# Performance work log

Measured on AMD Instinct MI355X. Metric: run time of the kernel, lower is better.

## Reference

```python
import jax, jax.numpy as jnp
from jax import lax
import numpy as np

H = 16  # GRU hidden = 4**N_GRAM * 4
V = 4   # 4**N_GRAM
B = 512
S = 8192


def _gru_cell(x, h, Wih, Whh, bih, bhh):
    # PyTorch GRU gate ordering: r, z, n
    gi = x @ Wih.T + bih          # [B, 3H]
    gh = h @ Whh.T + bhh          # [B, 3H]
    ir, iz, inn = jnp.split(gi, 3, axis=-1)
    hr, hz, hn = jnp.split(gh, 3, axis=-1)
    r = jax.nn.sigmoid(ir + hr)
    z = jax.nn.sigmoid(iz + hz)
    n = jnp.tanh(inn + r * hn)
    return (1.0 - z) * n + z * h


def setup_inputs() -> dict:
    key = jax.random.key(0)
    ks = jax.random.split(key, 12)
    f32 = jnp.float32
    k_i = 1.0 / np.sqrt(H)  # torch default GRU/Linear init scale
    u = lambda k, shp: jax.random.uniform(k, shp, f32, -k_i, k_i)
    gt = jax.random.normal(ks[0], (B, V, S), f32)
    return {
        "ground_truth": gt,
        "enc_Wih": u(ks[1], (3 * H, V)),
        "enc_Whh": u(ks[2], (3 * H, H)),
        "enc_bih": u(ks[3], (3 * H,)),
        "enc_bhh": u(ks[4], (3 * H,)),
        "dec_Wih": u(ks[5], (3 * H, V)),
        "dec_Whh": u(ks[6], (3 * H, H)),
        "dec_bih": u(ks[7], (3 * H,)),
        "dec_bhh": u(ks[8], (3 * H,)),
        "out_W": u(ks[9], (V, H)),
        "out_b": u(ks[10], (V,)),
        "emb": jnp.eye(V, dtype=f32),  # one-hot Embedding_LUT (frozen)
        "tf_rate": 1,
    }


def reference(ground_truth, enc_Wih, enc_Whh, enc_bih, enc_bhh,
              dec_Wih, dec_Whh, dec_bih, dec_bhh, out_W, out_b, emb, tf_rate):
    gt = jnp.transpose(ground_truth, (2, 0, 1))      # [S, B, V]
    seq_l, batch, _ = gt.shape
    dt = gt.dtype
    h0 = jnp.zeros((batch, H), dt)

    def enc_step(h, x):
        return _gru_cell(x, h, enc_Wih, enc_Whh, enc_bih, enc_bhh), None
    enc_hidden, _ = lax.scan(enc_step, h0, gt)

    targets = jnp.argmax(gt, axis=2)                 # [S, B] int
    x0 = jnp.zeros((batch, V), dt)
    loss0 = jnp.asarray(0.0, dt)

    if tf_rate >= 1:  # argmax-feedback branch (random() < tf_rate always true)
        def dec_step(carry, tgt):
            x, h, loss = carry
            h = _gru_cell(x, h, dec_Wih, dec_Whh, dec_bih, dec_bhh)
            out = h @ out_W.T + out_b                # [B, V]
            logp = jax.nn.log_softmax(out, axis=-1)
            nll = -jnp.mean(jnp.take_along_axis(logp, tgt[:, None], axis=1))
            top_i = jnp.argmax(out, axis=-1)
            return (emb[top_i], h, loss + nll), None
        (_, _, loss), _ = lax.scan(dec_step, (x0, enc_hidden, loss0), targets)
        output_batch = jnp.zeros((seq_l, batch, V), dt)  # never written in this branch
    else:  # teacher-forcing branch (NLLLoss applied to raw logits, as in source)
        def dec_step(carry, inp):
            x, h, loss = carry
            gt_t, tgt = inp
            h = _gru_cell(x, h, dec_Wih, dec_Whh, dec_bih, dec_bhh)
            out = h @ out_W.T + out_b
            nll = -jnp.mean(jnp.take_along_axis(out, tgt[:, None], axis=1))
            return (gt_t, h, loss + nll), out
        (_, _, loss), output_batch = lax.scan(dec_step, (x0, enc_hidden, loss0), (gt, targets))

    return loss, jnp.transpose(output_batch, (1, 2, 0))  # [B, V, S]
```

## Files before the change

### kernel.cpp

```cpp
#include <hip/hip_runtime.h>

#define S_LEN 8192
#define NH 16
#define NV 4
#define NB 512

typedef _Float16 h2 __attribute__((ext_vector_type(2)));

template<int R>
__device__ __forceinline__ float rotf(float v) {
    return __int_as_float(__builtin_amdgcn_mov_dpp(__float_as_int(v), 0x120 + R, 0xF, 0xF, true));
}
template<int R>
__device__ __forceinline__ h2 roth(h2 v) {
    int i;
    __builtin_memcpy(&i, &v, 4);
    i = __builtin_amdgcn_mov_dpp(i, 0x120 + R, 0xF, 0xF, true);
    h2 o;
    __builtin_memcpy(&o, &i, 4);
    return o;
}
__device__ __forceinline__ float qxor1(float v) {
    return __int_as_float(__builtin_amdgcn_mov_dpp(__float_as_int(v), 0xB1, 0xF, 0xF, true));
}
__device__ __forceinline__ float qxor2(float v) {
    return __int_as_float(__builtin_amdgcn_mov_dpp(__float_as_int(v), 0x4E, 0xF, 0xF, true));
}

__device__ __forceinline__ float fsig(float x) {
    return __builtin_amdgcn_rcpf(1.0f + __expf(-x));
}
__device__ __forceinline__ float frcp(float x) { return __builtin_amdgcn_rcpf(x); }
__device__ __forceinline__ float4 ld4(const float* p) { return *(const float4*)p; }

__device__ __forceinline__ h2 pkh(float a, float b) {
    auto t = __builtin_amdgcn_cvt_pkrtz(a, b);
    h2 o;
    __builtin_memcpy(&o, &t, 4);
    return o;
}

__device__ __forceinline__ float xor32f(float v, bool isLo) {
    float a = v, b = v;
    asm("v_permlane32_swap_b32 %0, %1" : "+v"(a), "+v"(b));
    return isLo ? b : a;
}

#define FILL_HP16(hp, h)                                      \
    do {                                                      \
        h2 p0_ = pkh((h), rotf<1>(h));                        \
        hp[0] = p0_;                                          \
        hp[1] = roth<2>(p0_);                                 \
        hp[2] = roth<4>(p0_);                                 \
        hp[3] = roth<6>(p0_);                                 \
        hp[4] = roth<8>(p0_);                                 \
        hp[5] = roth<10>(p0_);                                \
        hp[6] = roth<12>(p0_);                                \
        hp[7] = roth<14>(p0_);                                \
    } while (0)

__device__ __forceinline__ float dotd2(const h2* __restrict__ w, const h2* hp, float start) {
    float a = __builtin_amdgcn_fdot2(w[0], hp[0], start, false);
    float b = __builtin_amdgcn_fdot2(w[1], hp[1], 0.0f, false);
    a = __builtin_amdgcn_fdot2(w[2], hp[2], a, false);
    b = __builtin_amdgcn_fdot2(w[3], hp[3], b, false);
    a = __builtin_amdgcn_fdot2(w[4], hp[4], a, false);
    b = __builtin_amdgcn_fdot2(w[5], hp[5], b, false);
    a = __builtin_amdgcn_fdot2(w[6], hp[6], a, false);
    b = __builtin_amdgcn_fdot2(w[7], hp[7], b, false);
    return a + b;
}

__global__ __launch_bounds__(64, 1) void enc_kernel(
    const float* __restrict__ gt,
    const float* __restrict__ eWih, const float* __restrict__ eWhh,
    const float* __restrict__ ebih, const float* __restrict__ ebhh,
    float* __restrict__ hsc)
{
    const int lane = threadIdx.x;
    const int j    = lane & 15;
    const int b    = blockIdx.x * 4 + (lane >> 4);

    int probe = __builtin_amdgcn_mov_dpp(j, 0x121, 0xF, 0xF, true);
    const int sgn = (probe == ((j + 1) & 15)) ? 1 : -1;

    const float* gb = gt + (size_t)b * (NV * S_LEN);

    h2 ewr[8], ewz[8], ewn[8];
#pragma unroll
    for (int p = 0; p < 8; ++p) {
        int k0 = (j + sgn * (2 * p)) & 15;
        int k1 = (j + sgn * (2 * p + 1)) & 15;
        ewr[p] = (h2){(_Float16)eWhh[(0 * NH + j) * NH + k0], (_Float16)eWhh[(0 * NH + j) * NH + k1]};
        ewz[p] = (h2){(_Float16)eWhh[(1 * NH + j) * NH + k0], (_Float16)eWhh[(1 * NH + j) * NH + k1]};
        ewn[p] = (h2){(_Float16)eWhh[(2 * NH + j) * NH + k0], (_Float16)eWhh[(2 * NH + j) * NH + k1]};
    }
    float exr[NV], exz[NV], exn[NV];
#pragma unroll
    for (int v = 0; v < NV; ++v) {
        exr[v] = eWih[(0 * NH + j) * NV + v];
        exz[v] = eWih[(1 * NH + j) * NV + v];
        exn[v] = eWih[(2 * NH + j) * NV + v];
    }
    const float c_er  = ebih[j] + ebhh[j];
    const float c_ez  = ebih[NH + j] + ebhh[NH + j];
    const float c_ein = ebih[2 * NH + j];
    const float c_ehn = ebhh[2 * NH + j];

    float h = 0.0f;

    auto gru = [&](float ar, float az, float hn, float inn) {
        float r  = fsig(ar);
        float z  = fsig(az);
        float t2 = fmaf(-2.0f, z, 2.0f);
        float tb = fmaf(z, h, z - 1.0f);
        float y  = fmaf(r, hn, inn);
        float w2 = frcp(1.0f + __expf(-2.0f * y));
        h = fmaf(w2, t2, tb);
    };

    auto estep = [&](float x0, float x1, float x2, float x3) {
        float xr = fmaf(exr[0], x0, fmaf(exr[1], x1, fmaf(exr[2], x2, fmaf(exr[3], x3, c_er))));
        float xz = fmaf(exz[0], x0, fmaf(exz[1], x1, fmaf(exz[2], x2, fmaf(exz[3], x3, c_ez))));
        float xn = fmaf(exn[0], x0, fmaf(exn[1], x1, fmaf(exn[2], x2, fmaf(exn[3], x3, c_ein))));
        h2 hp[8];
        FILL_HP16(hp, h);
        float ar = dotd2(ewr, hp, xr);
        float az = dotd2(ewz, hp, xz);
        float hn = dotd2(ewn, hp, c_ehn);
        gru(ar, az, hn, xn);
    };

    {
        float4 A0 = ld4(gb + 0 * S_LEN), A1 = ld4(gb + 1 * S_LEN),
               A2 = ld4(gb + 2 * S_LEN), A3 = ld4(gb + 3 * S_LEN);
        float4 B0 = ld4(gb + 0 * S_LEN + 4), B1 = ld4(gb + 1 * S_LEN + 4),
               B2 = ld4(gb + 2 * S_LEN + 4), B3 = ld4(gb + 3 * S_LEN + 4);
        for (int t = 0; t < S_LEN; t += 8) {
            estep(A0.x, A1.x, A2.x, A3.x);
            estep(A0.y, A1.y, A2.y, A3.y);
            estep(A0.z, A1.z, A2.z, A3.z);
            estep(A0.w, A1.w, A2.w, A3.w);
            int ta = t + 8;  if (ta > S_LEN - 4) ta = S_LEN - 4;
            A0 = ld4(gb + 0 * S_LEN + ta); A1 = ld4(gb + 1 * S_LEN + ta);
            A2 = ld4(gb + 2 * S_LEN + ta); A3 = ld4(gb + 3 * S_LEN + ta);
            estep(B0.x, B1.x, B2.x, B3.x);
            estep(B0.y, B1.y, B2.y, B3.y);
            estep(B0.z, B1.z, B2.z, B3.z);
            estep(B0.w, B1.w, B2.w, B3.w);
            int tb2 = t + 12; if (tb2 > S_LEN - 4) tb2 = S_LEN - 4;
            B0 = ld4(gb + 0 * S_LEN + tb2); B1 = ld4(gb + 1 * S_LEN + tb2);
            B2 = ld4(gb + 2 * S_LEN + tb2); B3 = ld4(gb + 3 * S_LEN + tb2);
        }
    }

    hsc[(size_t)b * NH + j] = h;
}

__global__ __launch_bounds__(64, 1) void dec_kernel(
    const float* __restrict__ dWih, const float* __restrict__ dWhh,
    const float* __restrict__ dbih, const float* __restrict__ dbhh,
    const float* __restrict__ oW,  const float* __restrict__ ob,
    const float* __restrict__ hsc,
    float* __restrict__ outs)
{
    const int lane = threadIdx.x;
    const int j    = lane & 15;
    const int q    = j & 3;
    const int row  = lane >> 4;
    const bool isLo = (lane < 32);
    const int b    = blockIdx.x * 2 + (row & 1);

    int probe = __builtin_amdgcn_mov_dpp(j, 0x121, 0xF, 0xF, true);
    const int sgn = (probe == ((j + 1) & 15)) ? 1 : -1;

    const int gA = isLo ? 0 : 1;
    h2 wA[8], wB[8];
#pragma unroll
    for (int p = 0; p < 8; ++p) {
        int k0 = (j + sgn * (2 * p)) & 15;
        int k1 = (j + sgn * (2 * p + 1)) & 15;
        wA[p] = (h2){(_Float16)dWhh[(gA * NH + j) * NH + k0],
                     (_Float16)dWhh[(gA * NH + j) * NH + k1]};
        float w0 = isLo ? dWhh[(2 * NH + j) * NH + k0] : oW[q * NH + k0];
        float w1 = isLo ? dWhh[(2 * NH + j) * NH + k1] : oW[q * NH + k1];
        wB[p] = (h2){(_Float16)w0, (_Float16)w1};
    }
    const float bR  = dbih[j] + dbhh[j];
    const float bZ  = dbih[NH + j] + dbhh[NH + j];
    const float bNi = dbih[2 * NH + j];
    const float bHn = dbhh[2 * NH + j];
    const float biasA  = isLo ? bR  : bZ;
    const float startB = isLo ? bHn : ob[q];
    float SA[NV], KN[NV];
#pragma unroll
    for (int m = 0; m < NV; ++m) {
        int c = m ^ q;
        SA[m] = dWih[(gA * NH + j) * NV + c];
        KN[m] = bNi + dWih[(2 * NH + j) * NV + c];
    }

    float h = hsc[(size_t)b * NH + j];

    int oidx = (b << 15) + q;
    const bool storer = isLo && (j < 4);

    auto dstep = [&]() {
        h2 hp[8];
        FILL_HP16(hp, h);
        float aA  = dotd2(wA, hp, biasA);
        float aB  = dotd2(wB, hp, startB);
        float aBP = xor32f(aB, isLo);
        float hn  = isLo ? aB  : aBP;
        float oa  = isLo ? aBP : aB;
        if (storer) outs[oidx] = oa;
        oidx += 4;
        float ob_ = qxor1(oa);
        float oc_ = qxor2(oa);
        float od_ = qxor2(ob_);
        bool cA = ob_ > oa;  float mA = fmaxf(oa, ob_);
        bool cB = od_ > oc_; float mB = fmaxf(oc_, od_);
        bool hi_ = mB > mA;
        float KA  = hi_ ? (cB ? SA[3] : SA[2]) : (cA ? SA[1] : SA[0]);
        float KN_ = hi_ ? (cB ? KN[3] : KN[2]) : (cA ? KN[1] : KN[0]);
        float sg  = fsig(aA + KA);
        float sgP = xor32f(sg, isLo);
        float r   = isLo ? sg  : sgP;
        float z   = isLo ? sgP : sg;
        float y   = fmaf(r, hn, KN_);
        float w2  = frcp(1.0f + __expf(-2.0f * y));
        float t2  = fmaf(-2.0f, z, 2.0f);
        float tb  = fmaf(z, h, z - 1.0f);
        h = fmaf(w2, t2, tb);
    };

    {
        h2 hp[8];
        FILL_HP16(hp, h);
        float aA  = dotd2(wA, hp, biasA);
        float aB  = dotd2(wB, hp, startB);
        float aBP = xor32f(aB, isLo);
        float hn  = isLo ? aB : aBP;
        float sg  = fsig(aA);
        float sgP = xor32f(sg, isLo);
        float r   = isLo ? sg  : sgP;
        float z   = isLo ? sgP : sg;
        float y   = fmaf(r, hn, bNi);
        float w2  = frcp(1.0f + __expf(-2.0f * y));
        float t2  = fmaf(-2.0f, z, 2.0f);
        float tb  = fmaf(z, h, z - 1.0f);
        h = fmaf(w2, t2, tb);
    }
    for (int u = 0; u < S_LEN - 4; u += 4) {
        dstep(); dstep(); dstep(); dstep();
    }
    dstep(); dstep(); dstep();

    {
        h2 hp[8];
        FILL_HP16(hp, h);
        float aB  = dotd2(wB, hp, startB);
        float aBP = xor32f(aB, isLo);
        float oa  = isLo ? aBP : aB;
        if (storer) outs[oidx] = oa;
    }
}

__global__ __launch_bounds__(1024) void loss_kernel(
    const float* __restrict__ gt, float* __restrict__ outs, float* __restrict__ loss)
{
    int tid = blockIdx.x * 1024 + threadIdx.x;
    int t = tid & (S_LEN - 1);
    int b = tid >> 13;
    float4 o = *(const float4*)(outs + (size_t)tid * 4);
    const float* g = gt + (size_t)b * (NV * S_LEN) + t;
    float p0 = g[0], p1 = g[S_LEN], p2 = g[2 * S_LEN], p3 = g[3 * S_LEN];
    int tg = (p1 > p0) ? 1 : 0;  float bm = fmaxf(p0, p1);
    tg = (p2 > bm) ? 2 : tg;     bm = fmaxf(p2, bm);
    tg = (p3 > bm) ? 3 : tg;
    float vt = (tg & 1) ? ((tg & 2) ? o.w : o.y) : ((tg & 2) ? o.z : o.x);
    float mx = fmaxf(fmaxf(o.x, o.y), fmaxf(o.z, o.w));
    float ss = __expf(o.x - mx) + __expf(o.y - mx) + __expf(o.z - mx) + __expf(o.w - mx);
    float v  = (mx - vt) + __logf(ss);
    *(float4*)(outs + (size_t)tid * 4) = make_float4(0.f, 0.f, 0.f, 0.f);
#pragma unroll
    for (int d = 1; d < 64; d <<= 1) v += __shfl_xor(v, d, 64);
    __shared__ float sm[16];
    int w = threadIdx.x >> 6;
    if ((threadIdx.x & 63) == 0) sm[w] = v;
    __syncthreads();
    if (threadIdx.x < 16) {
        float s = sm[threadIdx.x];
#pragma unroll
        for (int d = 1; d < 16; d <<= 1) s += __shfl_xor(s, d, 64);
        if (threadIdx.x == 0) atomicAdd(loss, s * (1.0f / NB));
    }
}

extern "C" void kernel_launch(void* const* d_in, const int* in_sizes, int n_in,
                              void* d_out, int out_size, void* d_ws, size_t ws_size,
                              hipStream_t stream) {
    (void)in_sizes; (void)n_in; (void)ws_size; (void)out_size;
    const float* gt   = (const float*)d_in[0];
    const float* eWih = (const float*)d_in[1];
    const float* eWhh = (const float*)d_in[2];
    const float* ebih = (const float*)d_in[3];
    const float* ebhh = (const float*)d_in[4];
    const float* dWih = (const float*)d_in[5];
    const float* dWhh = (const float*)d_in[6];
    const float* dbih = (const float*)d_in[7];
    const float* dbhh = (const float*)d_in[8];
    const float* oW   = (const float*)d_in[9];
    const float* ob   = (const float*)d_in[10];

    float* out  = (float*)d_out;
    float* outs = out + 1;
    float* hsc  = (float*)d_ws;
    (void)hipMemsetAsync(d_out, 0, sizeof(float), stream);
    enc_kernel<<<NB / 4, 64, 0, stream>>>(gt, eWih, eWhh, ebih, ebhh, hsc);
    dec_kernel<<<NB / 2, 64, 0, stream>>>(dWih, dWhh, dbih, dbhh, oW, ob, hsc, outs);
    loss_kernel<<<(NB * S_LEN) / 1024, 1024, 0, stream>>>(gt, outs, out);
}
```

Measured before the change: 3.329 ms.

## Split encoder gates across wave halves and fold log2e into weights for exp2

The encoder now handles two batch rows per 64-lane wave instead of four. The low half computes the r gate and the hidden part of the n gate, and the high half computes the z gate and the input part of the n gate, exchanging results with a permlane32 swap. Input projections are folded into the fp16 dot products as extra packed lanes. Both kernels pre-scale weights by log2(e) so sigmoid and tanh use exp2 directly, removing a multiply from the serial recurrence. This doubles the encoder wave count and puts the input projection into fp16, which costs some precision.

```diff
diff --git a/kernel.cpp b/kernel.cpp
--- a/kernel.cpp
+++ b/kernel.cpp
@@ -6,6 +6,9 @@
 #define NB 512
 
 typedef _Float16 h2 __attribute__((ext_vector_type(2)));
+
+#define L2E  1.4426950408889634f
+#define L2E2 2.8853900817779268f
 
 template<int R>
 __device__ __forceinline__ float rotf(float v) {
@@ -27,10 +30,9 @@
     return __int_as_float(__builtin_amdgcn_mov_dpp(__float_as_int(v), 0x4E, 0xF, 0xF, true));
 }
 
-__device__ __forceinline__ float fsig(float x) {
-    return __builtin_amdgcn_rcpf(1.0f + __expf(-x));
-}
+__device__ __forceinline__ float fex2(float x) { return __builtin_amdgcn_exp2f(x); }
 __device__ __forceinline__ float frcp(float x) { return __builtin_amdgcn_rcpf(x); }
+__device__ __forceinline__ float fsig2(float x) { return frcp(1.0f + fex2(-x)); }
 __device__ __forceinline__ float4 ld4(const float* p) { return *(const float4*)p; }
 
 __device__ __forceinline__ h2 pkh(float a, float b) {
@@ -40,10 +42,9 @@
     return o;
 }
 
-__device__ __forceinline__ float xor32f(float v, bool isLo) {
-    float a = v, b = v;
-    asm("v_permlane32_swap_b32 %0, %1" : "+v"(a), "+v"(b));
-    return isLo ? b : a;
+__device__ __forceinline__ void bcast32(float v, float& lo, float& hi) {
+    lo = v; hi = v;
+    asm("v_permlane32_swap_b32 %0, %1" : "+v"(lo), "+v"(hi));
 }
 
 #define FILL_HP16(hp, h)                                      \
@@ -70,6 +71,19 @@
     b = __builtin_amdgcn_fdot2(w[7], hp[7], b, false);
     return a + b;
 }
+__device__ __forceinline__ float dotd2x(const h2* __restrict__ w, const h2* hp, float start) {
+    float a = __builtin_amdgcn_fdot2(w[0], hp[0], start, false);
+    float b = __builtin_amdgcn_fdot2(w[1], hp[1], 0.0f, false);
+    a = __builtin_amdgcn_fdot2(w[2], hp[2], a, false);
+    b = __builtin_amdgcn_fdot2(w[3], hp[3], b, false);
+    a = __builtin_amdgcn_fdot2(w[4], hp[4], a, false);
+    b = __builtin_amdgcn_fdot2(w[5], hp[5], b, false);
+    a = __builtin_amdgcn_fdot2(w[6], hp[6], a, false);
+    b = __builtin_amdgcn_fdot2(w[7], hp[7], b, false);
+    a = __builtin_amdgcn_fdot2(w[8], hp[8], a, false);
+    b = __builtin_amdgcn_fdot2(w[9], hp[9], b, false);
+    return a + b;
+}
 
 __global__ __launch_bounds__(64, 1) void enc_kernel(
     const float* __restrict__ gt,
@@ -79,56 +93,57 @@
 {
     const int lane = threadIdx.x;
     const int j    = lane & 15;
-    const int b    = blockIdx.x * 4 + (lane >> 4);
+    const int row  = lane >> 4;
+    const bool isLo = (lane < 32);
+    const int b    = blockIdx.x * 2 + (row & 1);
 
     int probe = __builtin_amdgcn_mov_dpp(j, 0x121, 0xF, 0xF, true);
     const int sgn = (probe == ((j + 1) & 15)) ? 1 : -1;
 
     const float* gb = gt + (size_t)b * (NV * S_LEN);
 
-    h2 ewr[8], ewz[8], ewn[8];
+    const int gA = isLo ? 0 : 1;
+    h2 wA[10], wB[10];
 #pragma unroll
     for (int p = 0; p < 8; ++p) {
         int k0 = (j + sgn * (2 * p)) & 15;
         int k1 = (j + sgn * (2 * p + 1)) & 15;
-        ewr[p] = (h2){(_Float16)eWhh[(0 * NH + j) * NH + k0], (_Float16)eWhh[(0 * NH + j) * NH + k1]};
-        ewz[p] = (h2){(_Float16)eWhh[(1 * NH + j) * NH + k0], (_Float16)eWhh[(1 * NH + j) * NH + k1]};
-        ewn[p] = (h2){(_Float16)eWhh[(2 * NH + j) * NH + k0], (_Float16)eWhh[(2 * NH + j) * NH + k1]};
-    }
-    float exr[NV], exz[NV], exn[NV];
-#pragma unroll
-    for (int v = 0; v < NV; ++v) {
-        exr[v] = eWih[(0 * NH + j) * NV + v];
-        exz[v] = eWih[(1 * NH + j) * NV + v];
-        exn[v] = eWih[(2 * NH + j) * NV + v];
-    }
-    const float c_er  = ebih[j] + ebhh[j];
-    const float c_ez  = ebih[NH + j] + ebhh[NH + j];
-    const float c_ein = ebih[2 * NH + j];
-    const float c_ehn = ebhh[2 * NH + j];
+        wA[p] = (h2){(_Float16)(L2E * eWhh[(gA * NH + j) * NH + k0]),
+                     (_Float16)(L2E * eWhh[(gA * NH + j) * NH + k1])};
+        float n0 = isLo ? (L2E2 * eWhh[(2 * NH + j) * NH + k0]) : 0.0f;
+        float n1 = isLo ? (L2E2 * eWhh[(2 * NH + j) * NH + k1]) : 0.0f;
+        wB[p] = (h2){(_Float16)n0, (_Float16)n1};
+    }
+#pragma unroll
+    for (int p = 0; p < 2; ++p) {
+        wA[8 + p] = (h2){(_Float16)(L2E * eWih[(gA * NH + j) * NV + 2 * p]),
+                         (_Float16)(L2E * eWih[(gA * NH + j) * NV + 2 * p + 1])};
+        float n0 = isLo ? 0.0f : (L2E2 * eWih[(2 * NH + j) * NV + 2 * p]);
+        float n1 = isLo ? 0.0f : (L2E2 * eWih[(2 * NH + j) * NV + 2 * p + 1]);
+        wB[8 + p] = (h2){(_Float16)n0, (_Float16)n1};
+    }
+    const float startA = L2E * (ebih[gA * NH + j] + ebhh[gA * NH + j]);
+    const float startB = isLo ? (L2E2 * ebhh[2 * NH + j]) : (L2E2 * ebih[2 * NH + j]);
 
     float h = 0.0f;
 
-    auto gru = [&](float ar, float az, float hn, float inn) {
-        float r  = fsig(ar);
-        float z  = fsig(az);
+    auto estep = [&](float x0, float x1, float x2, float x3) {
+        h2 hp[10];
+        FILL_HP16(hp, h);
+        hp[8] = pkh(x0, x1);
+        hp[9] = pkh(x2, x3);
+        float vA = dotd2x(wA, hp, startA);
+        float vB = dotd2x(wB, hp, startB);
+        float ar, az, hn, inn;
+        bcast32(vA, ar, az);
+        bcast32(vB, hn, inn);
+        float r  = fsig2(ar);
+        float z  = fsig2(az);
+        float y  = fmaf(r, hn, inn);
+        float w2 = fsig2(y);
         float t2 = fmaf(-2.0f, z, 2.0f);
         float tb = fmaf(z, h, z - 1.0f);
-        float y  = fmaf(r, hn, inn);
-        float w2 = frcp(1.0f + __expf(-2.0f * y));
         h = fmaf(w2, t2, tb);
-    };
-
-    auto estep = [&](float x0, float x1, float x2, float x3) {
-        float xr = fmaf(exr[0], x0, fmaf(exr[1], x1, fmaf(exr[2], x2, fmaf(exr[3], x3, c_er))));
-        float xz = fmaf(exz[0], x0, fmaf(exz[1], x1, fmaf(exz[2], x2, fmaf(exz[3], x3, c_ez))));
-        float xn = fmaf(exn[0], x0, fmaf(exn[1], x1, fmaf(exn[2], x2, fmaf(exn[3], x3, c_ein))));
-        h2 hp[8];
-        FILL_HP16(hp, h);
-        float ar = dotd2(ewr, hp, xr);
-        float az = dotd2(ewz, hp, xz);
-        float hn = dotd2(ewn, hp, c_ehn);
-        gru(ar, az, hn, xn);
     };
 
     {
@@ -154,7 +169,7 @@
         }
     }
 
-    hsc[(size_t)b * NH + j] = h;
+    if (isLo) hsc[(size_t)b * NH + j] = h;
 }
 
 __global__ __launch_bounds__(64, 1) void dec_kernel(
@@ -180,24 +195,22 @@
     for (int p = 0; p < 8; ++p) {
         int k0 = (j + sgn * (2 * p)) & 15;
         int k1 = (j + sgn * (2 * p + 1)) & 15;
-        wA[p] = (h2){(_Float16)dWhh[(gA * NH + j) * NH + k0],
-                     (_Float16)dWhh[(gA * NH + j) * NH + k1]};
-        float w0 = isLo ? dWhh[(2 * NH + j) * NH + k0] : oW[q * NH + k0];
-        float w1 = isLo ? dWhh[(2 * NH + j) * NH + k1] : oW[q * NH + k1];
+        wA[p] = (h2){(_Float16)(L2E * dWhh[(gA * NH + j) * NH + k0]),
+                     (_Float16)(L2E * dWhh[(gA * NH + j) * NH + k1])};
+        float w0 = isLo ? (L2E2 * dWhh[(2 * NH + j) * NH + k0]) : oW[q * NH + k0];
+        float w1 = isLo ? (L2E2 * dWhh[(2 * NH + j) * NH + k1]) : oW[q * NH + k1];
         wB[p] = (h2){(_Float16)w0, (_Float16)w1};
     }
-    const float bR  = dbih[j] + dbhh[j];
-    const float bZ  = dbih[NH + j] + dbhh[NH + j];
-    const float bNi = dbih[2 * NH + j];
-    const float bHn = dbhh[2 * NH + j];
-    const float biasA  = isLo ? bR  : bZ;
-    const float startB = isLo ? bHn : ob[q];
+    const float bNi  = dbih[2 * NH + j];
+    const float bNiS = L2E2 * bNi;
+    const float biasA  = L2E * (dbih[gA * NH + j] + dbhh[gA * NH + j]);
+    const float startB = isLo ? (L2E2 * dbhh[2 * NH + j]) : ob[q];
     float SA[NV], KN[NV];
 #pragma unroll
     for (int m = 0; m < NV; ++m) {
         int c = m ^ q;
-        SA[m] = dWih[(gA * NH + j) * NV + c];
-        KN[m] = bNi + dWih[(2 * NH + j) * NV + c];
+        SA[m] = L2E * dWih[(gA * NH + j) * NV + c];
+        KN[m] = L2E2 * (bNi + dWih[(2 * NH + j) * NV + c]);
     }
 
     float h = hsc[(size_t)b * NH + j];
@@ -208,11 +221,10 @@
     auto dstep = [&]() {
         h2 hp[8];
         FILL_HP16(hp, h);
-        float aA  = dotd2(wA, hp, biasA);
-        float aB  = dotd2(wB, hp, startB);
-        float aBP = xor32f(aB, isLo);
-        float hn  = isLo ? aB  : aBP;
-        float oa  = isLo ? aBP : aB;
+        float aA = dotd2(wA, hp, biasA);
+        float vB = dotd2(wB, hp, startB);
+        float hn, oa;
+        bcast32(vB, hn, oa);
         if (storer) outs[oidx] = oa;
         oidx += 4;
         float ob_ = qxor1(oa);
@@ -223,12 +235,11 @@
         bool hi_ = mB > mA;
         float KA  = hi_ ? (cB ? SA[3] : SA[2]) : (cA ? SA[1] : SA[0]);
         float KN_ = hi_ ? (cB ? KN[3] : KN[2]) : (cA ? KN[1] : KN[0]);
-        float sg  = fsig(aA + KA);
-        float sgP = xor32f(sg, isLo);
-        float r   = isLo ? sg  : sgP;
-        float z   = isLo ? sgP : sg;
+        float sg  = fsig2(aA + KA);
+        float r, z;
+        bcast32(sg, r, z);
         float y   = fmaf(r, hn, KN_);
-        float w2  = frcp(1.0f + __expf(-2.0f * y));
+        float w2  = fsig2(y);
         float t2  = fmaf(-2.0f, z, 2.0f);
         float tb  = fmaf(z, h, z - 1.0f);
         h = fmaf(w2, t2, tb);
@@ -237,18 +248,17 @@
     {
         h2 hp[8];
         FILL_HP16(hp, h);
-        float aA  = dotd2(wA, hp, biasA);
-        float aB  = dotd2(wB, hp, startB);
-        float aBP = xor32f(aB, isLo);
-        float hn  = isLo ? aB : aBP;
-        float sg  = fsig(aA);
-        float sgP = xor32f(sg, isLo);
-        float r   = isLo ? sg  : sgP;
-        float z   = isLo ? sgP : sg;
-        float y   = fmaf(r, hn, bNi);
-        float w2  = frcp(1.0f + __expf(-2.0f * y));
-        float t2  = fmaf(-2.0f, z, 2.0f);
-        float tb  = fmaf(z, h, z - 1.0f);
+        float aA = dotd2(wA, hp, biasA);
+        float vB = dotd2(wB, hp, startB);
+        float hn, oa;
+        bcast32(vB, hn, oa);
+        float sg = fsig2(aA);
+        float r, z;
+        bcast32(sg, r, z);
+        float y  = fmaf(r, hn, bNiS);
+        float w2 = fsig2(y);
+        float t2 = fmaf(-2.0f, z, 2.0f);
+        float tb = fmaf(z, h, z - 1.0f);
         h = fmaf(w2, t2, tb);
     }
     for (int u = 0; u < S_LEN - 4; u += 4) {
@@ -259,9 +269,9 @@
     {
         h2 hp[8];
         FILL_HP16(hp, h);
-        float aB  = dotd2(wB, hp, startB);
-        float aBP = xor32f(aB, isLo);
-        float oa  = isLo ? aBP : aB;
+        float vB = dotd2(wB, hp, startB);
+        float hn, oa;
+        bcast32(vB, hn, oa);
         if (storer) outs[oidx] = oa;
     }
 }
@@ -317,7 +327,7 @@
     float* outs = out + 1;
     float* hsc  = (float*)d_ws;
     (void)hipMemsetAsync(d_out, 0, sizeof(float), stream);
-    enc_kernel<<<NB / 4, 64, 0, stream>>>(gt, eWih, eWhh, ebih, ebhh, hsc);
+    enc_kernel<<<NB / 2, 64, 0, stream>>>(gt, eWih, eWhh, ebih, ebhh, hsc);
     dec_kernel<<<NB / 2, 64, 0, stream>>>(dWih, dWhh, dbih, dbhh, oW, ob, hsc, outs);
     loss_kernel<<<(NB * S_LEN) / 1024, 1024, 0, stream>>>(gt, outs, out);
 }
```

After: 3.054 ms. 8.2% less time.
